# Performance work log

Measured on AMD Instinct MI355X. Metric: run time of the kernel, lower is better.

## Reference

```python
import jax, jax.numpy as jnp
import numpy as np

N_BITS = 4            # W4A4 duquant-style fake quantization
BLOCK = 128           # rotation block size


def _round_ste(x):
    # straight-through rounding (matches round_ste used by LLM quantizers)
    return x + jax.lax.stop_gradient(jnp.round(x) - x)


def _block_rotate(x, R):
    # apply block-diagonal rotation along the last dim: x[..., F] -> x[..., F]
    *lead, F = x.shape
    B = R.shape[0]
    xr = jnp.einsum('...kb,bc->...kc', x.reshape(*lead, F // B, B), R)
    return xr.reshape(*lead, F)


def _fake_quant(x, R, n_bits):
    # rotate -> dynamic asymmetric uniform quant over last dim -> dequant -> de-rotate
    qmax = 2 ** n_bits - 1
    xr = _block_rotate(x, R)
    xmin = jnp.minimum(xr.min(axis=-1, keepdims=True), 0.0)
    xmax = jnp.maximum(xr.max(axis=-1, keepdims=True), 0.0)
    scale = jnp.clip((xmax - xmin) / qmax, 1e-5, None)
    zero_point = jax.lax.stop_gradient(jnp.round(-xmin / scale))
    xq = jnp.clip(_round_ste(xr / scale) + zero_point, 0.0, float(qmax))
    xdq = (xq - zero_point) * scale
    return _block_rotate(xdq, R.T)


def setup_inputs() -> dict:
    key = jax.random.key(0)
    k1, k2, k3 = jax.random.split(key, 3)
    x = jax.random.normal(k1, (4, 2048, 4096), dtype=jnp.float32)
    weight = jax.random.normal(k2, (4096, 4096), dtype=jnp.float32) * 0.02
    bias = jax.random.normal(k3, (4096,), dtype=jnp.float32) * 0.01
    # fixed orthogonal rotation matrix (DuQuant learned/constructed rotation)
    rng = np.random.default_rng(0)
    Rnp, _ = np.linalg.qr(rng.standard_normal((BLOCK, BLOCK)).astype(np.float32))
    R = jnp.asarray(Rnp, dtype=jnp.float32)
    return {"input": x, "weight": weight, "bias": bias, "R": R}


def reference(input, weight, bias, R):
    # act fake-quant (use_act_quant=True), weight fake-quant (use_weight_quant=True)
    x_q = _fake_quant(input, R, N_BITS)        # [B, S, Fin]
    w_q = _fake_quant(weight, R, N_BITS)       # [Fout, Fin], per-out-channel quant
    out = jnp.einsum('bsi,oi->bso', x_q, w_q) + bias
    return out
```

## Files before the change

kernel.cpp:

```cpp
#include <hip/hip_runtime.h>
#include <hip/hip_bf16.h>
#include <stdint.h>


typedef __bf16    bf16x8 __attribute__((ext_vector_type(8)));
typedef float     f32x4  __attribute__((ext_vector_type(4)));
typedef int       i32x4  __attribute__((ext_vector_type(4)));
typedef uint32_t  u32;
typedef uint32_t  u32x4  __attribute__((ext_vector_type(4)));

__device__ __forceinline__ void gload_lds16(const void* g, void* l) {
  __builtin_amdgcn_global_load_lds(
      (__attribute__((address_space(1))) void*)(g),
      (__attribute__((address_space(3))) void*)(l), 16, 0, 0);
}

__global__ __launch_bounds__(256)
void prep_rt(const float* __restrict__ R, unsigned short* __restrict__ RT3)
{
  const int tid = blockIdx.x * 256 + threadIdx.x;
  const int q  = tid & 7;
  const int l  = (tid >> 3) & 63;
  const int f  = (tid >> 9) & 7;
  const int ks = tid >> 12;
  const float v = R[(ks * 32 + (l >> 4) * 8 + q) * 128 + f * 16 + (l & 15)];
  __hip_bfloat16 h1 = __float2bfloat16(v);
  const float rem = v - __bfloat162float(h1);
  __hip_bfloat16 h2 = __float2bfloat16(rem);
  const float rem2 = rem - __bfloat162float(h2);
  __hip_bfloat16 h3 = __float2bfloat16(rem2);
  RT3[tid]          = *(unsigned short*)&h1;
  RT3[16384 + tid]  = *(unsigned short*)&h2;
  RT3[32768 + tid]  = *(unsigned short*)&h3;
}

#define FQ_TB  98304
#define FQ_SC  (98304 + 8 * 2560)

__global__ __launch_bounds__(512, 2)
void fq_rot1p(const float* __restrict__ X,
              const unsigned short* __restrict__ RT3,
              uint8_t* __restrict__ Q,
              float4* __restrict__ stats)
{
  __shared__ __align__(16) char lds[98304 + 8 * 2560 + 1664];

  const int t = threadIdx.x, lane = t & 63, wid = t >> 6;
  const size_t rowbase = (size_t)blockIdx.x * 16;
  const int colw = wid * 512;

#pragma unroll
  for (int i = 0; i < 12; ++i)
    gload_lds16((const char*)RT3 + i * 8192 + t * 16, lds + i * 8192 + t * 16);
  asm volatile("s_waitcnt vmcnt(0)" ::: "memory");
  __syncthreads();

  float* smin  = (float*)(lds + FQ_SC);
  float* smax  = (float*)(lds + FQ_SC + 512);
  float* rowsc = (float*)(lds + FQ_SC + 1024);
  float* rowzp = (float*)(lds + FQ_SC + 1088);
  int*   qsumL = (int*)  (lds + FQ_SC + 1152);

  const float* xbase = X + (rowbase + (lane & 15)) * 4096 + colw + (lane >> 4) * 8;

  f32x4 acc[4][8];
#pragma unroll
  for (int b = 0; b < 4; ++b)
#pragma unroll
    for (int f = 0; f < 8; ++f) acc[b][f] = (f32x4){0.f, 0.f, 0.f, 0.f};

#pragma unroll 1
  for (int kk = 0; kk < 4; ++kk) {
    union { bf16x8 v; unsigned short u[8]; } xh[4], xl[4], x2[4];
#pragma unroll
    for (int b = 0; b < 4; ++b) {
      const f32x4 lo = *(const f32x4*)(xbase + b * 128 + kk * 32);
      const f32x4 hi = *(const f32x4*)(xbase + b * 128 + kk * 32 + 4);
#pragma unroll
      for (int e = 0; e < 8; ++e) {
        const float xv = (e < 4) ? lo[e] : hi[e - 4];
        __hip_bfloat16 h1 = __float2bfloat16(xv);
        const float rm = xv - __bfloat162float(h1);
        __hip_bfloat16 h2 = __float2bfloat16(rm);
        const float rm2 = rm - __bfloat162float(h2);
        __hip_bfloat16 h3 = __float2bfloat16(rm2);
        xh[b].u[e] = *(unsigned short*)&h1;
        xl[b].u[e] = *(unsigned short*)&h2;
        x2[b].u[e] = *(unsigned short*)&h3;
      }
    }
#pragma unroll
    for (int f = 0; f < 8; ++f) {
      const int off = ((kk * 8 + f) * 64 + lane) * 16;
      const bf16x8 bh = *(const bf16x8*)(lds + off);
      const bf16x8 bl = *(const bf16x8*)(lds + 32768 + off);
      const bf16x8 b2 = *(const bf16x8*)(lds + 65536 + off);
#pragma unroll
      for (int b = 0; b < 4; ++b) {
        acc[b][f] = __builtin_amdgcn_mfma_f32_16x16x32_bf16(bh, xh[b].v, acc[b][f], 0, 0, 0);
        acc[b][f] = __builtin_amdgcn_mfma_f32_16x16x32_bf16(bh, xl[b].v, acc[b][f], 0, 0, 0);
        acc[b][f] = __builtin_amdgcn_mfma_f32_16x16x32_bf16(bh, x2[b].v, acc[b][f], 0, 0, 0);
        acc[b][f] = __builtin_amdgcn_mfma_f32_16x16x32_bf16(bl, xh[b].v, acc[b][f], 0, 0, 0);
        acc[b][f] = __builtin_amdgcn_mfma_f32_16x16x32_bf16(bl, xl[b].v, acc[b][f], 0, 0, 0);
        acc[b][f] = __builtin_amdgcn_mfma_f32_16x16x32_bf16(b2, xh[b].v, acc[b][f], 0, 0, 0);
      }
    }
  }

  float mn = 0.f, mx = 0.f;
#pragma unroll
  for (int b = 0; b < 4; ++b)
#pragma unroll
    for (int f = 0; f < 8; ++f)
#pragma unroll
      for (int r = 0; r < 4; ++r) {
        mn = fminf(mn, acc[b][f][r]);
        mx = fmaxf(mx, acc[b][f][r]);
      }
  mn = fminf(mn, __shfl_xor(mn, 16, 64));
  mn = fminf(mn, __shfl_xor(mn, 32, 64));
  mx = fmaxf(mx, __shfl_xor(mx, 16, 64));
  mx = fmaxf(mx, __shfl_xor(mx, 32, 64));
  if (lane < 16) { smin[wid * 16 + lane] = mn; smax[wid * 16 + lane] = mx; }
  __syncthreads();
  if (t < 16) {
    float m = 0.f, M = 0.f;
#pragma unroll
    for (int q = 0; q < 8; ++q) {
      m = fminf(m, smin[q * 16 + t]);
      M = fmaxf(M, smax[q * 16 + t]);
    }
    const float sc = fmaxf((M - m) / 15.0f, 1e-5f);
    rowsc[t] = sc;
    rowzp[t] = rintf(-m / sc);
  }
  __syncthreads();
  const float scale = rowsc[lane & 15];
  const float zp    = rowzp[lane & 15];

  u32* tw = (u32*)(lds + FQ_TB + wid * 2560);
  int qsum = 0;
#pragma unroll
  for (int b = 0; b < 4; ++b) {
#pragma unroll
    for (int f = 0; f < 8; ++f) {
      u32 pk = 0;
#pragma unroll
      for (int r = 0; r < 4; ++r) {
        const float qf = fminf(fmaxf(rintf(acc[b][f][r] / scale) + zp, 0.0f), 15.0f);
        const int qi = (int)qf;
        qsum += qi;
        pk |= (u32)qi << (8 * r);
      }
      tw[(lane & 15) * 40 + f * 4 + (lane >> 4)] = pk;
    }
#pragma unroll
    for (int rr = 0; rr < 2; ++rr) {
      const int row = rr * 8 + (lane >> 3);
      const int ch  = lane & 7;
      const u32x4 v = *(const u32x4*)&tw[row * 40 + ch * 4];
      *(u32x4*)(Q + (rowbase + row) * 4096 + colw + b * 128 + ch * 16) = v;
    }
  }

  qsum += __shfl_xor(qsum, 16, 64);
  qsum += __shfl_xor(qsum, 32, 64);
  if (lane < 16) qsumL[wid * 16 + lane] = qsum;
  __syncthreads();
  if (t < 16) {
    int S = 0;
#pragma unroll
    for (int q = 0; q < 8; ++q) S += qsumL[q * 16 + t];
    stats[rowbase + t] = make_float4(rowsc[t], rowzp[t], (float)S, 0.0f);
  }
}

__global__ __launch_bounds__(256)
void prep_cols(const float4* __restrict__ Wst, float* __restrict__ colS,
               float* __restrict__ colA, float* __restrict__ colB)
{
  const int n = blockIdx.x * 256 + threadIdx.x;
  const float4 w = Wst[n];
  colS[n] = w.x;
  colA[n] = w.x * w.z - 4096.0f * w.x * w.y;
  colB[n] = w.x * w.y;
}

#define NT 32

__global__ __launch_bounds__(512, 2)
void gemm256_8ph_i8(const uint8_t* __restrict__ Ap,
                    const uint8_t* __restrict__ Bp,
                    const float4* __restrict__ Xst,
                    const float* __restrict__ colS,
                    const float* __restrict__ colA,
                    const float* __restrict__ colB,
                    const float* __restrict__ bias,
                    float* __restrict__ C)
{
  __shared__ __align__(16) uint8_t lds[131072];
  char* ldsB = (char*)lds;
  const char* ldsc = (const char*)lds;

  const int tid  = threadIdx.x;
  const int lane = tid & 63;
  const int wid  = tid >> 6;
  const int wm   = wid >> 2;
  const int wn   = wid & 3;

  int bid = blockIdx.x;
  int nwg = gridDim.x;
  int swz = ((nwg & 7) == 0) ? ((bid & 7) * (nwg >> 3) + (bid >> 3)) : bid;
  const int bm = (swz >> 4) * 256;
  const int bn = (swz & 15) * 256;

  const int t16 = tid * 16;
  int stOff0, stOff1;
  {
    int Lb0 = t16;
    int Lb1 = t16 + 8192;
    int Lp0 = Lb0 ^ (((Lb0 >> 9) & 1) << 5);
    int Lp1 = Lb1 ^ (((Lb1 >> 9) & 1) << 5);
    int s0 = Lp0 >> 10, w0 = Lp0 & 1023;
    int s1 = Lp1 >> 10, w1 = Lp1 & 1023;
    int r0 = ((s0 >> 1) << 4) | (w0 >> 6);
    int k0 = ((s0 & 1) << 6) | (w0 & 63);
    int r1 = ((s1 >> 1) << 4) | (w1 >> 6);
    int k1 = ((s1 & 1) << 6) | (w1 & 63);
    stOff0 = r0 * 4096 + k0;
    stOff1 = r1 * 4096 + k1;
  }

  int swzw = (lane & 15) * 64 + (lane >> 4) * 16;
  swzw ^= ((swzw & 512) ? 32 : 0);

#define STAGE(GP, GROW, KT, SLOT) do {                                   \
    const uint8_t* _g = (GP) + ((size_t)(GROW)) * 4096 + (KT);           \
    gload_lds16(_g + stOff0, ldsB + (SLOT) + t16);                       \
    gload_lds16(_g + stOff1, ldsB + (SLOT) + 8192 + t16);                \
  } while (0)

  i32x4 acc[8][4];
#pragma unroll
  for (int i = 0; i < 8; ++i)
#pragma unroll
    for (int j = 0; j < 4; ++j) acc[i][j] = (i32x4){0, 0, 0, 0};

  STAGE(Bp, bn,       0, 32768);
  STAGE(Ap, bm,       0, 0);
  STAGE(Ap, bm + 128, 0, 16384);
  STAGE(Bp, bn + 128, 0, 49152);
  STAGE(Bp, bn,       128, 65536 + 32768);
  STAGE(Ap, bm,       128, 65536);
  STAGE(Ap, bm + 128, 128, 65536 + 16384);
  asm volatile("s_waitcnt vmcnt(6)" ::: "memory");
  __builtin_amdgcn_s_barrier();

  const int wmOff = wm * 16384;
  const int wnOff = (wn >> 1) * 16384 + (wn & 1) * 8192;

#define LDA(P, I, KK) (*(const i32x4*)((P) + ((I) * 2 + (KK)) * 1024))
#define LDB(P, J, KK) (*(const i32x4*)((P) + ((J) * 2 + (KK)) * 1024))

#define MF16(I0, A00, A01, I1, A10, A11)                                      \
  acc[I0][0] = __builtin_amdgcn_mfma_i32_16x16x64_i8(A00, b00, acc[I0][0], 0, 0, 0); \
  acc[I0][1] = __builtin_amdgcn_mfma_i32_16x16x64_i8(A00, b10, acc[I0][1], 0, 0, 0); \
  acc[I0][2] = __builtin_amdgcn_mfma_i32_16x16x64_i8(A00, b20, acc[I0][2], 0, 0, 0); \
  acc[I0][3] = __builtin_amdgcn_mfma_i32_16x16x64_i8(A00, b30, acc[I0][3], 0, 0, 0); \
  acc[I1][0] = __builtin_amdgcn_mfma_i32_16x16x64_i8(A10, b00, acc[I1][0], 0, 0, 0); \
  acc[I1][1] = __builtin_amdgcn_mfma_i32_16x16x64_i8(A10, b10, acc[I1][1], 0, 0, 0); \
  acc[I1][2] = __builtin_amdgcn_mfma_i32_16x16x64_i8(A10, b20, acc[I1][2], 0, 0, 0); \
  acc[I1][3] = __builtin_amdgcn_mfma_i32_16x16x64_i8(A10, b30, acc[I1][3], 0, 0, 0); \
  acc[I0][0] = __builtin_amdgcn_mfma_i32_16x16x64_i8(A01, b01, acc[I0][0], 0, 0, 0); \
  acc[I0][1] = __builtin_amdgcn_mfma_i32_16x16x64_i8(A01, b11, acc[I0][1], 0, 0, 0); \
  acc[I0][2] = __builtin_amdgcn_mfma_i32_16x16x64_i8(A01, b21, acc[I0][2], 0, 0, 0); \
  acc[I0][3] = __builtin_amdgcn_mfma_i32_16x16x64_i8(A01, b31, acc[I0][3], 0, 0, 0); \
  acc[I1][0] = __builtin_amdgcn_mfma_i32_16x16x64_i8(A11, b01, acc[I1][0], 0, 0, 0); \
  acc[I1][1] = __builtin_amdgcn_mfma_i32_16x16x64_i8(A11, b11, acc[I1][1], 0, 0, 0); \
  acc[I1][2] = __builtin_amdgcn_mfma_i32_16x16x64_i8(A11, b21, acc[I1][2], 0, 0, 0); \
  acc[I1][3] = __builtin_amdgcn_mfma_i32_16x16x64_i8(A11, b31, acc[I1][3], 0, 0, 0);

#define TILE(T, D) do {                                                       \
    const char* aP = ldsc + (D) * 65536 + wmOff + swzw;                       \
    const char* bP = ldsc + (D) * 65536 + 32768 + wnOff + swzw;               \
               \
    i32x4 b00 = LDB(bP, 0, 0), b01 = LDB(bP, 0, 1);                           \
    i32x4 b10 = LDB(bP, 1, 0), b11 = LDB(bP, 1, 1);                           \
    i32x4 b20 = LDB(bP, 2, 0), b21 = LDB(bP, 2, 1);                           \
    i32x4 b30 = LDB(bP, 3, 0), b31 = LDB(bP, 3, 1);                           \
    i32x4 a00 = LDA(aP, 0, 0), a01 = LDA(aP, 0, 1);                           \
    i32x4 a10 = LDA(aP, 1, 0), a11 = LDA(aP, 1, 1);                           \
    if ((T) + 1 < NT) STAGE(Bp, bn + 128, ((T) + 1) * 128, ((D) ^ 1) * 65536 + 49152); \
    __builtin_amdgcn_s_barrier();                                             \
    asm volatile("s_waitcnt lgkmcnt(0)" ::: "memory");                        \
    __builtin_amdgcn_s_setprio(1);                                            \
    MF16(0, a00, a01, 1, a10, a11);                                           \
    __builtin_amdgcn_s_setprio(0);                                            \
    __builtin_amdgcn_sched_barrier(0);                                        \
                                        \
    i32x4 a20 = LDA(aP, 2, 0), a21 = LDA(aP, 2, 1);                           \
    i32x4 a30 = LDA(aP, 3, 0), a31 = LDA(aP, 3, 1);                           \
    i32x4 a40 = LDA(aP, 4, 0), a41 = LDA(aP, 4, 1);                           \
    i32x4 a50 = LDA(aP, 5, 0), a51 = LDA(aP, 5, 1);                           \
    i32x4 a60 = LDA(aP, 6, 0), a61 = LDA(aP, 6, 1);                           \
    i32x4 a70 = LDA(aP, 7, 0), a71 = LDA(aP, 7, 1);                           \
    __builtin_amdgcn_s_barrier();                                             \
    asm volatile("s_waitcnt lgkmcnt(0)" ::: "memory");                        \
    __builtin_amdgcn_s_setprio(1);                                            \
    MF16(2, a20, a21, 3, a30, a31);                                           \
    __builtin_amdgcn_s_setprio(0);                                            \
    __builtin_amdgcn_sched_barrier(0);                                        \
                                       \
    if ((T) + 2 < NT) STAGE(Bp, bn, ((T) + 2) * 128, (D) * 65536 + 32768);    \
    __builtin_amdgcn_s_barrier();                                             \
    __builtin_amdgcn_s_setprio(1);                                            \
    MF16(4, a40, a41, 5, a50, a51);                                           \
    __builtin_amdgcn_s_setprio(0);                                            \
    __builtin_amdgcn_sched_barrier(0);                                        \
                                    \
    if ((T) + 2 < NT) {                                                       \
      STAGE(Ap, bm,       ((T) + 2) * 128, (D) * 65536);                      \
      STAGE(Ap, bm + 128, ((T) + 2) * 128, (D) * 65536 + 16384);              \
    }                                                                         \
    __builtin_amdgcn_s_barrier();                                             \
    __builtin_amdgcn_s_setprio(1);                                            \
    MF16(6, a60, a61, 7, a70, a71);                                           \
    __builtin_amdgcn_s_setprio(0);                                            \
    if ((T) + 2 < NT)      { asm volatile("s_waitcnt vmcnt(6)" ::: "memory"); } \
    else if ((T) + 1 < NT) { asm volatile("s_waitcnt vmcnt(0)" ::: "memory"); } \
    __builtin_amdgcn_sched_barrier(0);                                        \
        \
    __builtin_amdgcn_s_barrier();                                             \
  } while (0)

  for (int t = 0; t < NT; t += 2) {
    TILE(t, 0);
    TILE(t + 1, 1);
  }

  {
    float* tile = (float*)ldsB;
    const int P = 268;
#pragma unroll 1
    for (int quarter = 0; quarter < 4; ++quarter) {
      __builtin_amdgcn_s_barrier();
      if (wm == (quarter >> 1)) {
        const int qi0 = (quarter & 1) * 4;
#pragma unroll
        for (int i = 0; i < 4; ++i)
#pragma unroll
          for (int j = 0; j < 4; ++j) {
            const int rl = i * 16 + (lane >> 4) * 4;
            const int cl = wn * 64 + j * 16 + (lane & 15);
#pragma unroll
            for (int r = 0; r < 4; ++r)
              tile[(rl + r) * P + cl] = (float)acc[qi0 + i][j][r];
          }
      }
      __builtin_amdgcn_s_barrier();
#pragma unroll 1
      for (int rr = 0; rr < 8; ++rr) {
        const int rl = wid * 8 + rr;
        const int grow = bm + quarter * 64 + rl;
        const float4 xs4 = Xst[grow];
        const float r1 = xs4.x, r2 = xs4.x * xs4.y, r3 = xs4.x * xs4.z;
        const int n0 = bn + lane * 4;
        const f32x4 v  = *(const f32x4*)&tile[rl * P + lane * 4];
        const f32x4 cs = *(const f32x4*)&colS[n0];
        const f32x4 ca = *(const f32x4*)&colA[n0];
        const f32x4 cb = *(const f32x4*)&colB[n0];
        const f32x4 bi = *(const f32x4*)&bias[n0];
        f32x4 o;
#pragma unroll
        for (int e = 0; e < 4; ++e)
          o[e] = r1 * cs[e] * v[e] - r2 * ca[e] - r3 * cb[e] + bi[e];
        __builtin_nontemporal_store(o, (f32x4*)&C[(size_t)grow * 4096 + n0]);
      }
    }
  }
#undef TILE
#undef MF16
#undef LDA
#undef LDB
#undef STAGE
}

extern "C" void kernel_launch(void* const* d_in, const int* in_sizes, int n_in,
                              void* d_out, int out_size, void* d_ws, size_t ws_size,
                              hipStream_t stream)
{
  const float* x    = (const float*)d_in[0];
  const float* wgt  = (const float*)d_in[1];
  const float* bias = (const float*)d_in[2];
  const float* R    = (const float*)d_in[3];

  const int K = 4096, N = 4096;
  const int M = in_sizes[0] / K;

  uint8_t* Qx = (uint8_t*)d_ws;
  uint8_t* Qw = Qx + (size_t)M * K;
  float4*  Sx = (float4*)(Qw + (size_t)N * K);
  float4*  Sw = Sx + M;
  unsigned short* RT3 = (unsigned short*)(Sw + N);
  float* colS = (float*)((char*)RT3 + 98304);
  float* colA = colS + N;
  float* colB = colA + N;

  prep_rt<<<64, 256, 0, stream>>>(R, RT3);
  fq_rot1p<<<M / 16, 512, 0, stream>>>(x,   RT3, Qx, Sx);
  fq_rot1p<<<N / 16, 512, 0, stream>>>(wgt, RT3, Qw, Sw);
  prep_cols<<<N / 256, 256, 0, stream>>>(Sw, colS, colA, colB);

  const int nblk = (M / 256) * (N / 256);
  gemm256_8ph_i8<<<nblk, 512, 0, stream>>>(Qx, Qw, Sx, colS, colA, colB, bias,
                                           (float*)d_out);
}
```

Baseline: 288.9 us.

## Pack 4-bit quantized codes two per byte and unpack in GEMM

The quantize kernel now packs two 4-bit codes into each byte, halving the Q buffers for activations and weights. The GEMM stages half as many bytes per K-tile into LDS (smaller LDS footprint, fewer global loads) and unpacks nibbles with mask/shift into int8 operands before the MFMAs. This cuts global and LDS traffic at the cost of extra VALU unpack work in the inner loop, which sits between the barrier and the MFMAs. The smaller LDS allocation may also allow higher occupancy.

After: 296.6 us. 2.7% more time.

```diff
diff --git a/kernel.cpp b/kernel.cpp
--- a/kernel.cpp
+++ b/kernel.cpp
@@ -35,7 +35,7 @@
 }
 
 #define FQ_TB  98304
-#define FQ_SC  (98304 + 8 * 2560)
+#define FQ_SC  (98304 + 8 * 1280)
 
 __global__ __launch_bounds__(512, 2)
 void fq_rot1p(const float* __restrict__ X,
@@ -43,11 +43,12 @@
               uint8_t* __restrict__ Q,
               float4* __restrict__ stats)
 {
-  __shared__ __align__(16) char lds[98304 + 8 * 2560 + 1664];
+  __shared__ __align__(16) char lds[98304 + 8 * 1280 + 1664];
 
   const int t = threadIdx.x, lane = t & 63, wid = t >> 6;
   const size_t rowbase = (size_t)blockIdx.x * 16;
-  const int colw = wid * 512;
+  const int colw  = wid * 512;
+  const int colwp = wid * 256;
 
 #pragma unroll
   for (int i = 0; i < 12; ++i)
@@ -138,29 +139,27 @@
   const float scale = rowsc[lane & 15];
   const float zp    = rowzp[lane & 15];
 
-  u32* tw = (u32*)(lds + FQ_TB + wid * 2560);
+  u32* tw = (u32*)(lds + FQ_TB + wid * 1280);
   int qsum = 0;
 #pragma unroll
   for (int b = 0; b < 4; ++b) {
+    u32 pk[4] = {0u, 0u, 0u, 0u};
 #pragma unroll
     for (int f = 0; f < 8; ++f) {
-      u32 pk = 0;
 #pragma unroll
       for (int r = 0; r < 4; ++r) {
         const float qf = fminf(fmaxf(rintf(acc[b][f][r] / scale) + zp, 0.0f), 15.0f);
         const int qi = (int)qf;
         qsum += qi;
-        pk |= (u32)qi << (8 * r);
-      }
-      tw[(lane & 15) * 40 + f * 4 + (lane >> 4)] = pk;
+        pk[r] |= (u32)qi << (8 * (f & 3) + 4 * (f >> 2));
+      }
     }
 #pragma unroll
-    for (int rr = 0; rr < 2; ++rr) {
-      const int row = rr * 8 + (lane >> 3);
-      const int ch  = lane & 7;
-      const u32x4 v = *(const u32x4*)&tw[row * 40 + ch * 4];
-      *(u32x4*)(Q + (rowbase + row) * 4096 + colw + b * 128 + ch * 16) = v;
-    }
+    for (int r = 0; r < 4; ++r)
+      tw[(lane & 15) * 20 + (lane >> 4) * 4 + r] = pk[r];
+    const int row = lane >> 2, ch = lane & 3;
+    const u32x4 v = *(const u32x4*)&tw[row * 20 + ch * 4];
+    *(u32x4*)(Q + (rowbase + row) * 2048 + colwp + b * 64 + ch * 16) = v;
   }
 
   qsum += __shfl_xor(qsum, 16, 64);
@@ -198,7 +197,7 @@
                     const float* __restrict__ bias,
                     float* __restrict__ C)
 {
-  __shared__ __align__(16) uint8_t lds[131072];
+  __shared__ __align__(16) uint8_t lds[68608];
   char* ldsB = (char*)lds;
   const char* ldsc = (const char*)lds;
 
@@ -215,30 +214,19 @@
   const int bn = (swz & 15) * 256;
 
   const int t16 = tid * 16;
-  int stOff0, stOff1;
+  int stOff;
   {
-    int Lb0 = t16;
-    int Lb1 = t16 + 8192;
-    int Lp0 = Lb0 ^ (((Lb0 >> 9) & 1) << 5);
-    int Lp1 = Lb1 ^ (((Lb1 >> 9) & 1) << 5);
-    int s0 = Lp0 >> 10, w0 = Lp0 & 1023;
-    int s1 = Lp1 >> 10, w1 = Lp1 & 1023;
-    int r0 = ((s0 >> 1) << 4) | (w0 >> 6);
-    int k0 = ((s0 & 1) << 6) | (w0 & 63);
-    int r1 = ((s1 >> 1) << 4) | (w1 >> 6);
-    int k1 = ((s1 & 1) << 6) | (w1 & 63);
-    stOff0 = r0 * 4096 + k0;
-    stOff1 = r1 * 4096 + k1;
+    int Lp = t16 ^ (((t16 >> 9) & 1) << 5);
+    int s = Lp >> 10, w = Lp & 1023;
+    stOff = (((s << 4) | (w >> 6)) * 2048) + (w & 63);
   }
 
   int swzw = (lane & 15) * 64 + (lane >> 4) * 16;
   swzw ^= ((swzw & 512) ? 32 : 0);
 
-#define STAGE(GP, GROW, KT, SLOT) do {                                   \
-    const uint8_t* _g = (GP) + ((size_t)(GROW)) * 4096 + (KT);           \
-    gload_lds16(_g + stOff0, ldsB + (SLOT) + t16);                       \
-    gload_lds16(_g + stOff1, ldsB + (SLOT) + 8192 + t16);                \
-  } while (0)
+#define STAGE(GP, GROW, KTP, SLOT)                                       \
+    gload_lds16((GP) + ((size_t)(GROW)) * 2048 + (KTP) + stOff,          \
+                ldsB + (SLOT) + t16)
 
   i32x4 acc[8][4];
 #pragma unroll
@@ -246,21 +234,26 @@
 #pragma unroll
     for (int j = 0; j < 4; ++j) acc[i][j] = (i32x4){0, 0, 0, 0};
 
-  STAGE(Bp, bn,       0, 32768);
+  STAGE(Bp, bn,       0, 16384);
   STAGE(Ap, bm,       0, 0);
-  STAGE(Ap, bm + 128, 0, 16384);
-  STAGE(Bp, bn + 128, 0, 49152);
-  STAGE(Bp, bn,       128, 65536 + 32768);
-  STAGE(Ap, bm,       128, 65536);
-  STAGE(Ap, bm + 128, 128, 65536 + 16384);
-  asm volatile("s_waitcnt vmcnt(6)" ::: "memory");
+  STAGE(Ap, bm + 128, 0, 8192);
+  STAGE(Bp, bn + 128, 0, 24576);
+  STAGE(Bp, bn,       64, 32768 + 16384);
+  STAGE(Ap, bm,       64, 32768);
+  STAGE(Ap, bm + 128, 64, 32768 + 8192);
+  asm volatile("s_waitcnt vmcnt(3)" ::: "memory");
   __builtin_amdgcn_s_barrier();
 
-  const int wmOff = wm * 16384;
-  const int wnOff = (wn >> 1) * 16384 + (wn & 1) * 8192;
-
-#define LDA(P, I, KK) (*(const i32x4*)((P) + ((I) * 2 + (KK)) * 1024))
-#define LDB(P, J, KK) (*(const i32x4*)((P) + ((J) * 2 + (KK)) * 1024))
+  const int aOff = wm * 8192;
+  const int bOff = 16384 + (wn >> 1) * 8192 + (wn & 1) * 4096;
+
+#define LD1(P, I) (*(const i32x4*)((P) + (I) * 1024))
+#define UNPK(P, LO, HI) do {                                                  \
+    _Pragma("unroll")                                                         \
+    for (int _e = 0; _e < 4; ++_e) {                                          \
+      (LO)[_e] = (P)[_e] & 0x0F0F0F0F;                                        \
+      (HI)[_e] = ((P)[_e] >> 4) & 0x0F0F0F0F;                                 \
+    } } while (0)
 
 #define MF16(I0, A00, A01, I1, A10, A11)                                      \
   acc[I0][0] = __builtin_amdgcn_mfma_i32_16x16x64_i8(A00, b00, acc[I0][0], 0, 0, 0); \
@@ -281,37 +274,37 @@
   acc[I1][3] = __builtin_amdgcn_mfma_i32_16x16x64_i8(A11, b31, acc[I1][3], 0, 0, 0);
 
 #define TILE(T, D) do {                                                       \
-    const char* aP = ldsc + (D) * 65536 + wmOff + swzw;                       \
-    const char* bP = ldsc + (D) * 65536 + 32768 + wnOff + swzw;               \
-               \
-    i32x4 b00 = LDB(bP, 0, 0), b01 = LDB(bP, 0, 1);                           \
-    i32x4 b10 = LDB(bP, 1, 0), b11 = LDB(bP, 1, 1);                           \
-    i32x4 b20 = LDB(bP, 2, 0), b21 = LDB(bP, 2, 1);                           \
-    i32x4 b30 = LDB(bP, 3, 0), b31 = LDB(bP, 3, 1);                           \
-    i32x4 a00 = LDA(aP, 0, 0), a01 = LDA(aP, 0, 1);                           \
-    i32x4 a10 = LDA(aP, 1, 0), a11 = LDA(aP, 1, 1);                           \
-    if ((T) + 1 < NT) STAGE(Bp, bn + 128, ((T) + 1) * 128, ((D) ^ 1) * 65536 + 49152); \
+    const char* aP = ldsc + (D) * 32768 + aOff + swzw;                        \
+    const char* bP = ldsc + (D) * 32768 + bOff + swzw;                        \
+         \
+    i32x4 pb0 = LD1(bP, 0), pb1 = LD1(bP, 1);                                 \
+    i32x4 pb2 = LD1(bP, 2), pb3 = LD1(bP, 3);                                 \
+    i32x4 pa0 = LD1(aP, 0), pa1 = LD1(aP, 1);                                 \
+    if ((T) + 1 < NT) STAGE(Bp, bn + 128, ((T) + 1) * 64, ((D) ^ 1) * 32768 + 24576); \
     __builtin_amdgcn_s_barrier();                                             \
     asm volatile("s_waitcnt lgkmcnt(0)" ::: "memory");                        \
+    i32x4 b00, b01, b10, b11, b20, b21, b30, b31, a00, a01, a10, a11;         \
+    UNPK(pb0, b00, b01); UNPK(pb1, b10, b11);                                 \
+    UNPK(pb2, b20, b21); UNPK(pb3, b30, b31);                                 \
+    UNPK(pa0, a00, a01); UNPK(pa1, a10, a11);                                 \
     __builtin_amdgcn_s_setprio(1);                                            \
     MF16(0, a00, a01, 1, a10, a11);                                           \
     __builtin_amdgcn_s_setprio(0);                                            \
     __builtin_amdgcn_sched_barrier(0);                                        \
                                         \
-    i32x4 a20 = LDA(aP, 2, 0), a21 = LDA(aP, 2, 1);                           \
-    i32x4 a30 = LDA(aP, 3, 0), a31 = LDA(aP, 3, 1);                           \
-    i32x4 a40 = LDA(aP, 4, 0), a41 = LDA(aP, 4, 1);                           \
-    i32x4 a50 = LDA(aP, 5, 0), a51 = LDA(aP, 5, 1);                           \
-    i32x4 a60 = LDA(aP, 6, 0), a61 = LDA(aP, 6, 1);                           \
-    i32x4 a70 = LDA(aP, 7, 0), a71 = LDA(aP, 7, 1);                           \
+    i32x4 pa2 = LD1(aP, 2), pa3 = LD1(aP, 3), pa4 = LD1(aP, 4);               \
+    i32x4 pa5 = LD1(aP, 5), pa6 = LD1(aP, 6), pa7 = LD1(aP, 7);               \
     __builtin_amdgcn_s_barrier();                                             \
     asm volatile("s_waitcnt lgkmcnt(0)" ::: "memory");                        \
+    i32x4 a20, a21, a30, a31, a40, a41, a50, a51, a60, a61, a70, a71;         \
+    UNPK(pa2, a20, a21); UNPK(pa3, a30, a31); UNPK(pa4, a40, a41);            \
+    UNPK(pa5, a50, a51); UNPK(pa6, a60, a61); UNPK(pa7, a70, a71);            \
     __builtin_amdgcn_s_setprio(1);                                            \
     MF16(2, a20, a21, 3, a30, a31);                                           \
     __builtin_amdgcn_s_setprio(0);                                            \
     __builtin_amdgcn_sched_barrier(0);                                        \
                                        \
-    if ((T) + 2 < NT) STAGE(Bp, bn, ((T) + 2) * 128, (D) * 65536 + 32768);    \
+    if ((T) + 2 < NT) STAGE(Bp, bn, ((T) + 2) * 64, (D) * 32768 + 16384);     \
     __builtin_amdgcn_s_barrier();                                             \
     __builtin_amdgcn_s_setprio(1);                                            \
     MF16(4, a40, a41, 5, a50, a51);                                           \
@@ -319,14 +312,14 @@
     __builtin_amdgcn_sched_barrier(0);                                        \
                                     \
     if ((T) + 2 < NT) {                                                       \
-      STAGE(Ap, bm,       ((T) + 2) * 128, (D) * 65536);                      \
-      STAGE(Ap, bm + 128, ((T) + 2) * 128, (D) * 65536 + 16384);              \
+      STAGE(Ap, bm,       ((T) + 2) * 64, (D) * 32768);                       \
+      STAGE(Ap, bm + 128, ((T) + 2) * 64, (D) * 32768 + 8192);                \
     }                                                                         \
     __builtin_amdgcn_s_barrier();                                             \
     __builtin_amdgcn_s_setprio(1);                                            \
     MF16(6, a60, a61, 7, a70, a71);                                           \
     __builtin_amdgcn_s_setprio(0);                                            \
-    if ((T) + 2 < NT)      { asm volatile("s_waitcnt vmcnt(6)" ::: "memory"); } \
+    if ((T) + 2 < NT)      { asm volatile("s_waitcnt vmcnt(3)" ::: "memory"); } \
     else if ((T) + 1 < NT) { asm volatile("s_waitcnt vmcnt(0)" ::: "memory"); } \
     __builtin_amdgcn_sched_barrier(0);                                        \
         \
@@ -380,8 +373,8 @@
   }
 #undef TILE
 #undef MF16
-#undef LDA
-#undef LDB
+#undef UNPK
+#undef LD1
 #undef STAGE
 }
 
@@ -398,8 +391,8 @@
   const int M = in_sizes[0] / K;
 
   uint8_t* Qx = (uint8_t*)d_ws;
-  uint8_t* Qw = Qx + (size_t)M * K;
-  float4*  Sx = (float4*)(Qw + (size_t)N * K);
+  uint8_t* Qw = Qx + (size_t)M * 2048;
+  float4*  Sx = (float4*)(Qw + (size_t)N * 2048);
   float4*  Sw = Sx + M;
   unsigned short* RT3 = (unsigned short*)(Sw + N);
   float* colS = (float*)((char*)RT3 + 98304);
```
